# Kernel tuning notes

Measured on AMD Instinct MI355X. Metric: run time of the kernel, lower is better.

The kernel has to match this reference:

```python
import jax, jax.numpy as jnp
import numpy as np
import math

H = 16
D_MODEL = 1024
D_K = D_MODEL // H


def setup_inputs() -> dict:
    key = jax.random.key(0)
    ks = jax.random.split(key, 11)
    B, S = 2, 2048
    scale = 1.0 / math.sqrt(D_MODEL)
    inp = {
        "query": jax.random.normal(ks[0], (B, S, D_MODEL), dtype=jnp.float32),
        "key": jax.random.normal(ks[1], (B, S, D_MODEL), dtype=jnp.float32),
        "value": jax.random.normal(ks[2], (B, S, D_MODEL), dtype=jnp.float32),
        # torch nn.Linear convention: W is [out_features, in_features]
        "Wq": jax.random.normal(ks[3], (D_MODEL, D_MODEL), dtype=jnp.float32) * scale,
        "bq": jnp.zeros((D_MODEL,), dtype=jnp.float32),
        "Wk": jax.random.normal(ks[4], (D_MODEL, D_MODEL), dtype=jnp.float32) * scale,
        "bk": jnp.zeros((D_MODEL,), dtype=jnp.float32),
        "Wv": jax.random.normal(ks[5], (D_MODEL, D_MODEL), dtype=jnp.float32) * scale,
        "bv": jnp.zeros((D_MODEL,), dtype=jnp.float32),
        "Wo": jax.random.normal(ks[6], (D_MODEL, D_MODEL), dtype=jnp.float32) * scale,
        "bo": jnp.zeros((D_MODEL,), dtype=jnp.float32),
    }
    return inp


def _split_heads(x):
    # [b, s, h*d_k] -> [b, h, s, d_k]
    b, s, _ = x.shape
    return x.reshape(b, s, H, D_K).transpose(0, 2, 1, 3)


def reference(query, key, value, Wq, bq, Wk, bk, Wv, bv, Wo, bo):
    q = _split_heads(query @ Wq.T + bq)
    k = _split_heads(key @ Wk.T + bk)
    v = _split_heads(value @ Wv.T + bv)
    # scaled dot-product attention, full L x L scores per head
    scores = jnp.einsum("bhqd,bhkd->bhqk", q, k) / math.sqrt(D_K)
    attn = jax.nn.softmax(scores, axis=-1)
    ctx = jnp.einsum("bhqk,bhkd->bhqd", attn, v)  # [b, h, s, d_k]
    b, h, s, d = ctx.shape
    ctx = ctx.transpose(0, 2, 1, 3).reshape(b, s, h * d)
    return ctx @ Wo.T + bo
```

## Files before the change

kernel.cpp:

```cpp
#include <hip/hip_runtime.h>

typedef unsigned int u32;
typedef unsigned short u16;
typedef __attribute__((ext_vector_type(8))) short short8;
typedef __attribute__((ext_vector_type(4))) float f32x4;
typedef __attribute__((ext_vector_type(2))) u32 u32x2;
typedef __attribute__((ext_vector_type(4))) u32 u32x4;

#define DEV __device__ __forceinline__

DEV u16 f2bf(float f) {
  u32 u = __builtin_bit_cast(u32, f);
  u = (u + 0x7FFFu + ((u >> 16) & 1u)) >> 16;
  return (u16)u;
}

DEV float fexp2(float x) {
#if __has_builtin(__builtin_amdgcn_exp2f)
  return __builtin_amdgcn_exp2f(x);
#else
  return exp2f(x);
#endif
}

DEV u32 cvt_pk_bf16(float lo, float hi) {
  u32 r;
  asm("v_cvt_pk_bf16_f32 %0, %1, %2" : "=v"(r) : "v"(lo), "v"(hi));
  return r;
}

DEV void llds16(const void* g, void* lds) {
  __builtin_amdgcn_global_load_lds(
      (const __attribute__((address_space(1))) u32*)g,
      (__attribute__((address_space(3))) u32*)lds, 16, 0, 0);
}

struct CvtW {
  const float* src[4];
  u16* dst[4];
};

__global__ void cvt_w(CvtW cw) {
  int i = blockIdx.x * blockDim.x + threadIdx.x;
  int seg = i >> 17;
  size_t off = ((size_t)(i & 131071)) * 8;
  const f32x4* p = (const f32x4*)(cw.src[seg] + off);
  f32x4 a = p[0], b = p[1];
  u32x4 o;
  o[0] = cvt_pk_bf16(a[0], a[1]);
  o[1] = cvt_pk_bf16(a[2], a[3]);
  o[2] = cvt_pk_bf16(b[0], b[1]);
  o[3] = cvt_pk_bf16(b[2], b[3]);
  *(u32x4*)(cw.dst[seg] + off) = o;
}

struct GemmArgs {
  const void* A[3];
  const u16* W[3];
  const float* bias[3];
  void* C[3];
  float scale[3];
};

template <int BM, int BN, int WAVES_M, int OUT_BF16, int NB_M, int A_F32>
__global__ __launch_bounds__(256, 2) void gemm_bt(GemmArgs ga) {
  constexpr int K = 1024, N = 1024;
  constexpr int WAVES_N = 4 / WAVES_M;
  constexpr int WM = BM / WAVES_M, WN = BN / WAVES_N;
  constexpr int AM = WM / 16, AN = WN / 16;

  __shared__ u16 lsA[BM * 32];
  __shared__ u16 lsB[BN * 32];

  const u32 orig = blockIdx.x;
  const u32 nid = (orig & 7u) * (gridDim.x >> 3) + (orig >> 3);
  const int bn = (int)(nid & 7u);
  const int bm = (int)((nid >> 3) % (u32)NB_M);
  const int z = (int)((nid >> 3) / (u32)NB_M);

  const u16* __restrict__ W = ga.W[z];
  const int tid = threadIdx.x;
  const int l = tid & 63, w = tid >> 6;
  const int lg = l >> 4, lr = l & 15;
  const int wm = w / WAVES_N, wn = w % WAVES_N;

  f32x4 acc[AM][AN];
#pragma unroll
  for (int i = 0; i < AM; ++i)
#pragma unroll
    for (int j = 0; j < AN; ++j) acc[i][j] = (f32x4){0.f, 0.f, 0.f, 0.f};

  for (int k0 = 0; k0 < K; k0 += 32) {
    __syncthreads();
    if constexpr (A_F32) {
      const float* __restrict__ Af = (const float*)ga.A[z];
#pragma unroll
      for (int i = 0; i < BN / 64; ++i) {
        u32 sb = (u32)(w * (BN / 64) + i) * 1024;
        u32 lb = sb + l * 16;
        u32 row = lb >> 6, colS = (lb & 63) >> 1;
        llds16(W + (size_t)(bn * BN + row) * K + k0 + colS, (char*)lsB + sb);
      }
      {
        constexpr int TPR = 256 / BM;
        int row = tid / TPR, kh = tid % TPR;
        const f32x4* src = (const f32x4*)(Af + (size_t)(bm * BM + row) * K + k0 + kh * 16);
        f32x4 f0 = src[0], f1 = src[1], f2 = src[2], f3 = src[3];
        u32x4 o0, o1;
        o0[0] = cvt_pk_bf16(f0[0], f0[1]); o0[1] = cvt_pk_bf16(f0[2], f0[3]);
        o0[2] = cvt_pk_bf16(f1[0], f1[1]); o0[3] = cvt_pk_bf16(f1[2], f1[3]);
        o1[0] = cvt_pk_bf16(f2[0], f2[1]); o1[1] = cvt_pk_bf16(f2[2], f2[3]);
        o1[2] = cvt_pk_bf16(f3[0], f3[1]); o1[3] = cvt_pk_bf16(f3[2], f3[3]);
        char* dst = (char*)lsA + row * 64 + kh * 32;
        *(u32x4*)dst = o0;
        *(u32x4*)(dst + 16) = o1;
      }
    } else {
      const u16* __restrict__ A = (const u16*)ga.A[z];
      constexpr int SEGS = (BM + BN) / 16;
      constexpr int PW = SEGS / 4;
#pragma unroll
      for (int i = 0; i < PW; ++i) {
        int s = w * PW + i;
        if (s < BM / 16) {
          u32 sb = s * 1024;
          u32 lb = sb + l * 16;
          u32 row = lb >> 6, colS = (lb & 63) >> 1;
          llds16(A + (size_t)(bm * BM + row) * K + k0 + colS, (char*)lsA + sb);
        } else {
          u32 sb = (u32)(s - BM / 16) * 1024;
          u32 lb = sb + l * 16;
          u32 row = lb >> 6, colS = (lb & 63) >> 1;
          llds16(W + (size_t)(bn * BN + row) * K + k0 + colS, (char*)lsB + sb);
        }
      }
    }
    __syncthreads();
    short8 af[AM], bf[AN];
#pragma unroll
    for (int i = 0; i < AM; ++i)
      af[i] = *(const short8*)&lsA[(wm * WM + i * 16 + lr) * 32 + lg * 8];
#pragma unroll
    for (int j = 0; j < AN; ++j)
      bf[j] = *(const short8*)&lsB[(wn * WN + j * 16 + lr) * 32 + lg * 8];
#pragma unroll
    for (int i = 0; i < AM; ++i)
#pragma unroll
      for (int j = 0; j < AN; ++j)
        acc[i][j] = __builtin_amdgcn_mfma_f32_16x16x32_bf16(af[i], bf[j], acc[i][j], 0, 0, 0);
  }

  const float sc = ga.scale[z];
  const float* __restrict__ bias = ga.bias[z];
#pragma unroll
  for (int j = 0; j < AN; ++j) {
    int col = bn * BN + wn * WN + j * 16 + lr;
    float bv = bias[col];
#pragma unroll
    for (int i = 0; i < AM; ++i) {
      int row0 = bm * BM + wm * WM + i * 16 + lg * 4;
#pragma unroll
      for (int r = 0; r < 4; ++r) {
        float v = (acc[i][j][r] + bv) * sc;
        if constexpr (OUT_BF16)
          ((u16*)ga.C[z])[(size_t)(row0 + r) * N + col] = f2bf(v);
        else
          ((float*)ga.C[z])[(size_t)(row0 + r) * N + col] = v;
      }
    }
  }
}

__global__ __launch_bounds__(256, 2) void attn_fwd(
    const u16* __restrict__ Q, const u16* __restrict__ Kp,
    const u16* __restrict__ V, u16* __restrict__ O) {
  constexpr int S = 2048, LD = 1024;
  __shared__ u16 Kt[4][64 * 64];
  __shared__ u16 Vt[4][64 * 64];
  const int tid = threadIdx.x;
  const int l = tid & 63, w = tid >> 6;
  const int lg = l >> 4, lr = l & 15;

  const u32 orig = blockIdx.x;
  const u32 nid = (orig & 7u) * 64u + (orig >> 3);
  const int qt = (int)(nid & 15u);
  const int h = (int)((nid >> 4) & 15u);
  const int b = (int)(nid >> 8);

  const size_t base = ((size_t)b * S) * LD + h * 64;
  const int q0 = qt * 128 + w * 32;

  short8 qf[2][2];
#pragma unroll
  for (int g = 0; g < 2; ++g)
#pragma unroll
    for (int c = 0; c < 2; ++c)
      qf[g][c] = *(const short8*)&Q[base + (size_t)(q0 + g * 16 + lr) * LD + c * 32 + lg * 8];

  f32x4 acc[2][4];
#pragma unroll
  for (int g = 0; g < 2; ++g)
#pragma unroll
    for (int i = 0; i < 4; ++i) acc[g][i] = (f32x4){0.f, 0.f, 0.f, 0.f};
  float lsum[2] = {0.f, 0.f};

  const int m = tid & 31;
  const int kp0 = m * 2;
  const int key0 = ((m & 16) << 1) + ((m & 2) << 3) + (((m >> 2) & 3) << 2) + ((m & 1) << 1);
  const int vd0 = (tid >> 5) * 8;

#define KSTAGE(T)                                                               \
  {                                                                             \
    _Pragma("unroll") for (int i_ = 0; i_ < 2; ++i_) {                          \
      u32 sb = (u32)(w * 2 + i_) * 1024;                                        \
      u32 lb = sb + l * 16;                                                     \
      u32 key = lb >> 7;                                                        \
      u32 inner = (lb & 127) ^ ((key & 7) << 4);                                \
      llds16(Kp + base + (size_t)((T) * 64 + key) * LD + (inner >> 1),          \
             (char*)Kt[(T) & 3] + sb);                                          \
    }                                                                           \
  }
#define VLOAD(T, VA, VB)                                                        \
  {                                                                             \
    VA = *(const short8*)&V[base + (size_t)((T) * 64 + key0) * LD + vd0];       \
    VB = *(const short8*)&V[base + (size_t)((T) * 64 + key0 + 1) * LD + vd0];   \
  }
#define VWRITE(T, VA, VB)                                                       \
  {                                                                             \
    _Pragma("unroll") for (int jj = 0; jj < 8; ++jj) {                          \
      u32 pv = (u32)(u16)(VA)[jj] | ((u32)(u16)(VB)[jj] << 16);                 \
      u32 addr = (u32)((vd0 + jj) * 128 + kp0 * 2) ^ ((u32)jj << 4);            \
      *(u32*)((char*)Vt[(T) & 3] + addr) = pv;                                  \
    }                                                                           \
  }
#define QK(T, SV)                                                               \
  {                                                                             \
    __builtin_amdgcn_s_setprio(1);                                              \
    _Pragma("unroll") for (int ks = 0; ks < 4; ++ks) {                          \
      u32 a0 = (u32)(((ks * 16 + lr) * 128 + lg * 16) ^ ((lr & 7) << 4));       \
      short8 kf0 = *(const short8*)((const char*)Kt[(T) & 3] + a0);             \
      short8 kf1 = *(const short8*)((const char*)Kt[(T) & 3] + (a0 ^ 64));      \
      _Pragma("unroll") for (int g = 0; g < 2; ++g) {                           \
        f32x4 s_ = (f32x4){0.f, 0.f, 0.f, 0.f};                                 \
        s_ = __builtin_amdgcn_mfma_f32_16x16x32_bf16(kf0, qf[g][0], s_, 0, 0, 0); \
        s_ = __builtin_amdgcn_mfma_f32_16x16x32_bf16(kf1, qf[g][1], s_, 0, 0, 0); \
        SV[g][ks] = s_;                                                         \
      }                                                                         \
    }                                                                           \
    __builtin_amdgcn_s_setprio(0);                                              \
  }
#define SM(SV, PK)                                                              \
  {                                                                             \
    _Pragma("unroll") for (int g = 0; g < 2; ++g) {                             \
      _Pragma("unroll") for (int ks = 0; ks < 4; ++ks) {                        \
        float e0 = fexp2(SV[g][ks][0]), e1 = fexp2(SV[g][ks][1]);               \
        float e2 = fexp2(SV[g][ks][2]), e3 = fexp2(SV[g][ks][3]);               \
        lsum[g] += (e0 + e1) + (e2 + e3);                                       \
        PK[g][ks * 2 + 0] = cvt_pk_bf16(e0, e1);                                \
        PK[g][ks * 2 + 1] = cvt_pk_bf16(e2, e3);                                \
      }                                                                         \
    }                                                                           \
  }
#define PV(T, PK)                                                               \
  {                                                                             \
    __builtin_amdgcn_s_setprio(1);                                              \
    _Pragma("unroll") for (int ds = 0; ds < 4; ++ds) {                          \
      _Pragma("unroll") for (int c = 0; c < 2; ++c) {                           \
        u32 va_ = (u32)(((ds * 16 + lr) * 128 + c * 64 + lg * 16) ^ ((lr & 7) << 4)); \
        short8 vf = *(const short8*)((const char*)Vt[(T) & 3] + va_);           \
        _Pragma("unroll") for (int g = 0; g < 2; ++g) {                         \
          u32x4 pc = {PK[g][c * 4 + 0], PK[g][c * 4 + 1], PK[g][c * 4 + 2], PK[g][c * 4 + 3]}; \
          short8 pf = __builtin_bit_cast(short8, pc);                           \
          acc[g][ds] = __builtin_amdgcn_mfma_f32_16x16x32_bf16(vf, pf, acc[g][ds], 0, 0, 0); \
        }                                                                       \
      }                                                                         \
    }                                                                           \
    __builtin_amdgcn_s_setprio(0);                                              \
  }
#define ITER(t, SVC, SVN, VCA, VCB, VNA, VNB)                                   \
  {                                                                             \
    if ((t) < 30) { VLOAD((t) + 2, VNA, VNB); KSTAGE((t) + 2); }                \
    if ((t) < 31) QK((t) + 1, SVN);                                             \
    u32 pk_[2][8];                                                              \
    SM(SVC, pk_);                                                               \
    if ((t) < 31) VWRITE((t) + 1, VCA, VCB);                                    \
    PV(t, pk_);                                                                 \
    __syncthreads();                                                            \
  }

  f32x4 svA[2][4], svB[2][4];
  short8 vaA, vbA, vaB, vbB;

  VLOAD(0, vaB, vbB); KSTAGE(0);
  VLOAD(1, vaA, vbA); KSTAGE(1);
  VWRITE(0, vaB, vbB);
  __syncthreads();
  QK(0, svA);

  for (int tt = 0; tt < 16; ++tt) {
    ITER(2 * tt, svA, svB, vaA, vbA, vaB, vbB);
    ITER(2 * tt + 1, svB, svA, vaB, vbB, vaA, vbA);
  }

#pragma unroll
  for (int g = 0; g < 2; ++g) {
    lsum[g] += __shfl_xor(lsum[g], 16);
    lsum[g] += __shfl_xor(lsum[g], 32);
  }
#pragma unroll
  for (int g = 0; g < 2; ++g) {
    float inv = __builtin_amdgcn_rcpf(lsum[g]);
#pragma unroll
    for (int ds = 0; ds < 4; ++ds) {
      u32x2 ov;
      ov[0] = cvt_pk_bf16(acc[g][ds][0] * inv, acc[g][ds][1] * inv);
      ov[1] = cvt_pk_bf16(acc[g][ds][2] * inv, acc[g][ds][3] * inv);
      *(u32x2*)&O[base + (size_t)(q0 + g * 16 + lr) * LD + ds * 16 + lg * 4] = ov;
    }
  }
#undef KSTAGE
#undef VLOAD
#undef VWRITE
#undef QK
#undef SM
#undef PV
#undef ITER
}

extern "C" void kernel_launch(void* const* d_in, const int* in_sizes, int n_in,
                              void* d_out, int out_size, void* d_ws, size_t ws_size,
                              hipStream_t stream) {
  constexpr size_t SZ_X = 4096ull * 1024;
  constexpr size_t SZ_W = 1024ull * 1024;
  const float* bq = (const float*)d_in[4];
  const float* bk = (const float*)d_in[6];
  const float* bv = (const float*)d_in[8];
  const float* bo = (const float*)d_in[10];

  char* ws = (char*)d_ws;
  u16* wqb = (u16*)ws;
  u16* wkb = wqb + SZ_W;
  u16* wvb = wkb + SZ_W;
  u16* wob = wvb + SZ_W;
  u16* Qp = wob + SZ_W;
  u16* Kp = Qp + SZ_X;
  u16* Vp = Kp + SZ_X;
  u16* Cx = Vp + SZ_X;

  CvtW cw;
  cw.src[0] = (const float*)d_in[3]; cw.dst[0] = wqb;
  cw.src[1] = (const float*)d_in[5]; cw.dst[1] = wkb;
  cw.src[2] = (const float*)d_in[7]; cw.dst[2] = wvb;
  cw.src[3] = (const float*)d_in[9]; cw.dst[3] = wob;
  cvt_w<<<dim3(2048), 256, 0, stream>>>(cw);

  GemmArgs g1;
  g1.A[0] = d_in[0]; g1.A[1] = d_in[1]; g1.A[2] = d_in[2];
  g1.W[0] = wqb; g1.W[1] = wkb; g1.W[2] = wvb;
  g1.bias[0] = bq; g1.bias[1] = bk; g1.bias[2] = bv;
  g1.C[0] = Qp; g1.C[1] = Kp; g1.C[2] = Vp;
  g1.scale[0] = 0.18033688011112042f;
  g1.scale[1] = 1.f; g1.scale[2] = 1.f;
  gemm_bt<128, 128, 2, 1, 32, 1><<<dim3(768), 256, 0, stream>>>(g1);

  attn_fwd<<<dim3(512), 256, 0, stream>>>(Qp, Kp, Vp, Cx);

  GemmArgs g2 = {};
  g2.A[0] = Cx; g2.W[0] = wob; g2.bias[0] = bo; g2.C[0] = d_out; g2.scale[0] = 1.f;
  gemm_bt<64, 128, 1, 0, 64, 0><<<dim3(512), 256, 0, stream>>>(g2);
}
```

Before: 131.2 us.

## Swizzle GEMM LDS layout and register-prefetch fp32 A tiles one step ahead

Applies an XOR swizzle on the 16-byte column chunks of the A and B LDS tiles, keyed on the row, on both the direct-to-LDS loads and the fragment reads, so the MFMA fragment loads hit fewer bank conflicts. In the fp32-A path, the next K-step's A values are loaded into registers before the current step converts and stores its own, so global-load latency overlaps the MFMA work. This raises register pressure, and the fp32 path now assumes a fixed 2-segment-per-wave layout, i.e. BM=128 and BN=128.

Result: faster. 123.6 us (-5.8%).

```diff
diff --git a/kernel.cpp b/kernel.cpp
--- a/kernel.cpp
+++ b/kernel.cpp
@@ -90,65 +90,105 @@
 #pragma unroll
     for (int j = 0; j < AN; ++j) acc[i][j] = (f32x4){0.f, 0.f, 0.f, 0.f};
 
-  for (int k0 = 0; k0 < K; k0 += 32) {
-    __syncthreads();
-    if constexpr (A_F32) {
-      const float* __restrict__ Af = (const float*)ga.A[z];
-#pragma unroll
-      for (int i = 0; i < BN / 64; ++i) {
-        u32 sb = (u32)(w * (BN / 64) + i) * 1024;
-        u32 lb = sb + l * 16;
-        u32 row = lb >> 6, colS = (lb & 63) >> 1;
-        llds16(W + (size_t)(bn * BN + row) * K + k0 + colS, (char*)lsB + sb);
-      }
-      {
-        constexpr int TPR = 256 / BM;
-        int row = tid / TPR, kh = tid % TPR;
-        const f32x4* src = (const f32x4*)(Af + (size_t)(bm * BM + row) * K + k0 + kh * 16);
-        f32x4 f0 = src[0], f1 = src[1], f2 = src[2], f3 = src[3];
-        u32x4 o0, o1;
-        o0[0] = cvt_pk_bf16(f0[0], f0[1]); o0[1] = cvt_pk_bf16(f0[2], f0[3]);
-        o0[2] = cvt_pk_bf16(f1[0], f1[1]); o0[3] = cvt_pk_bf16(f1[2], f1[3]);
-        o1[0] = cvt_pk_bf16(f2[0], f2[1]); o1[1] = cvt_pk_bf16(f2[2], f2[3]);
-        o1[2] = cvt_pk_bf16(f3[0], f3[1]); o1[3] = cvt_pk_bf16(f3[2], f3[3]);
-        char* dst = (char*)lsA + row * 64 + kh * 32;
-        *(u32x4*)dst = o0;
-        *(u32x4*)(dst + 16) = o1;
-      }
-    } else {
-      const u16* __restrict__ A = (const u16*)ga.A[z];
-      constexpr int SEGS = (BM + BN) / 16;
-      constexpr int PW = SEGS / 4;
+#define WDMA_SWZ(NSEG)                                                          \
+  {                                                                             \
+    _Pragma("unroll") for (int i_ = 0; i_ < (NSEG); ++i_) {                     \
+      u32 sb = (u32)(w * (NSEG) + i_) * 1024;                                   \
+      u32 lbw = sb + l * 16;                                                    \
+      u32 row = lbw >> 6;                                                       \
+      u32 colB = (lbw & 63) ^ ((row & 3) << 4);                                 \
+      llds16(W + (size_t)(bn * BN + row) * K + k0 + (colB >> 1),                \
+             (char*)lsB + sb);                                                  \
+    }                                                                           \
+  }
+#define FRAG_MFMA()                                                             \
+  {                                                                             \
+    short8 af[AM], bf[AN];                                                      \
+    _Pragma("unroll") for (int i = 0; i < AM; ++i) {                            \
+      u32 ar = (u32)(wm * WM + i * 16 + lr);                                    \
+      af[i] = *(const short8*)((const char*)lsA + ar * 64 +                     \
+                               ((u32)(lg * 16) ^ ((ar & 3) << 4)));             \
+    }                                                                           \
+    _Pragma("unroll") for (int j = 0; j < AN; ++j) {                            \
+      u32 br = (u32)(wn * WN + j * 16 + lr);                                    \
+      bf[j] = *(const short8*)((const char*)lsB + br * 64 +                     \
+                               ((u32)(lg * 16) ^ ((br & 3) << 4)));             \
+    }                                                                           \
+    _Pragma("unroll") for (int i = 0; i < AM; ++i)                              \
+    _Pragma("unroll") for (int j = 0; j < AN; ++j)                              \
+      acc[i][j] = __builtin_amdgcn_mfma_f32_16x16x32_bf16(af[i], bf[j],         \
+                                                          acc[i][j], 0, 0, 0); \
+  }
+
+  if constexpr (A_F32) {
+    const float* __restrict__ Af = (const float*)ga.A[z];
+    const u32 lb0 = (u32)(w * 2 + 0) * 1024 + l * 16;
+    const u32 lb1 = (u32)(w * 2 + 1) * 1024 + l * 16;
+    const u32 sw0 = lb0 ^ (((lb0 >> 6) & 3) << 4);
+    const u32 sw1 = lb1 ^ (((lb1 >> 6) & 3) << 4);
+    const float* src0 = Af + (size_t)(bm * BM + (lb0 >> 6)) * K + ((lb0 & 63) >> 1);
+    const float* src1 = Af + (size_t)(bm * BM + (lb1 >> 6)) * K + ((lb1 & 63) >> 1);
+
+    f32x4 cA0, cA1, cB0, cB1, nA0, nA1, nB0, nB1;
+    cA0 = *(const f32x4*)src0; cA1 = *(const f32x4*)(src0 + 4);
+    cB0 = *(const f32x4*)src1; cB1 = *(const f32x4*)(src1 + 4);
+
+#define GSTEP(K0, CA0, CA1, CB0, CB1, NA0, NA1, NB0, NB1)                       \
+  {                                                                             \
+    const int k0 = (K0);                                                        \
+    __syncthreads();                                                            \
+    if (k0 + 32 < K) {          \
+      NA0 = *(const f32x4*)(src0 + k0 + 32); NA1 = *(const f32x4*)(src0 + k0 + 36); \
+      NB0 = *(const f32x4*)(src1 + k0 + 32); NB1 = *(const f32x4*)(src1 + k0 + 36); \
+    }                                                                           \
+    WDMA_SWZ(2);                                                                \
+    {                                                                           \
+      u32x4 o;                                                                  \
+      o[0] = cvt_pk_bf16(CA0[0], CA0[1]); o[1] = cvt_pk_bf16(CA0[2], CA0[3]);   \
+      o[2] = cvt_pk_bf16(CA1[0], CA1[1]); o[3] = cvt_pk_bf16(CA1[2], CA1[3]);   \
+      *(u32x4*)((char*)lsA + sw0) = o;                                          \
+      o[0] = cvt_pk_bf16(CB0[0], CB0[1]); o[1] = cvt_pk_bf16(CB0[2], CB0[3]);   \
+      o[2] = cvt_pk_bf16(CB1[0], CB1[1]); o[3] = cvt_pk_bf16(CB1[2], CB1[3]);   \
+      *(u32x4*)((char*)lsA + sw1) = o;                                          \
+    }                                                                           \
+    __syncthreads();                                                            \
+    FRAG_MFMA();                                                                \
+  }
+
+    for (int kk = 0; kk < K; kk += 64) {
+      GSTEP(kk, cA0, cA1, cB0, cB1, nA0, nA1, nB0, nB1);
+      GSTEP(kk + 32, nA0, nA1, nB0, nB1, cA0, cA1, cB0, cB1);
+    }
+#undef GSTEP
+  } else {
+    const u16* __restrict__ A = (const u16*)ga.A[z];
+    constexpr int SEGS = (BM + BN) / 16;
+    constexpr int PW = SEGS / 4;
+    for (int k0 = 0; k0 < K; k0 += 32) {
+      __syncthreads();
 #pragma unroll
       for (int i = 0; i < PW; ++i) {
         int s = w * PW + i;
         if (s < BM / 16) {
           u32 sb = s * 1024;
           u32 lb = sb + l * 16;
-          u32 row = lb >> 6, colS = (lb & 63) >> 1;
-          llds16(A + (size_t)(bm * BM + row) * K + k0 + colS, (char*)lsA + sb);
+          u32 row = lb >> 6;
+          u32 colB = (lb & 63) ^ ((row & 3) << 4);
+          llds16(A + (size_t)(bm * BM + row) * K + k0 + (colB >> 1), (char*)lsA + sb);
         } else {
           u32 sb = (u32)(s - BM / 16) * 1024;
           u32 lb = sb + l * 16;
-          u32 row = lb >> 6, colS = (lb & 63) >> 1;
-          llds16(W + (size_t)(bn * BN + row) * K + k0 + colS, (char*)lsB + sb);
+          u32 row = lb >> 6;
+          u32 colB = (lb & 63) ^ ((row & 3) << 4);
+          llds16(W + (size_t)(bn * BN + row) * K + k0 + (colB >> 1), (char*)lsB + sb);
         }
       }
+      __syncthreads();
+      FRAG_MFMA();
     }
-    __syncthreads();
-    short8 af[AM], bf[AN];
-#pragma unroll
-    for (int i = 0; i < AM; ++i)
-      af[i] = *(const short8*)&lsA[(wm * WM + i * 16 + lr) * 32 + lg * 8];
-#pragma unroll
-    for (int j = 0; j < AN; ++j)
-      bf[j] = *(const short8*)&lsB[(wn * WN + j * 16 + lr) * 32 + lg * 8];
-#pragma unroll
-    for (int i = 0; i < AM; ++i)
-#pragma unroll
-      for (int j = 0; j < AN; ++j)
-        acc[i][j] = __builtin_amdgcn_mfma_f32_16x16x32_bf16(af[i], bf[j], acc[i][j], 0, 0, 0);
-  }
+  }
+#undef WDMA_SWZ
+#undef FRAG_MFMA
 
   const float sc = ga.scale[z];
   const float* __restrict__ bias = ga.bias[z];
```

## Double K tile to 64 with XOR-swizzled LDS and register-prefetched fp32 A

Applied to the files above, without the earlier changes.

Raises the GEMM K-step from 32 to 64, which halves the number of barrier pairs per tile. LDS rows are now 128 bytes with an XOR swizzle on the row index to avoid bank conflicts. In the fp32-input path, the next A tile is loaded into registers while the current one is converted and computed on, hiding global load latency. This doubles LDS use and raises register pressure, which may reduce occupancy at 2 blocks per CU.

Measured after the change: 127.6 us. -2.7%, faster.

```diff
diff --git a/kernel.cpp b/kernel.cpp
--- a/kernel.cpp
+++ b/kernel.cpp
@@ -69,8 +69,8 @@
   constexpr int WM = BM / WAVES_M, WN = BN / WAVES_N;
   constexpr int AM = WM / 16, AN = WN / 16;
 
-  __shared__ u16 lsA[BM * 32];
-  __shared__ u16 lsB[BN * 32];
+  __shared__ u16 lsA[BM * 64];
+  __shared__ u16 lsB[BN * 64];
 
   const u32 orig = blockIdx.x;
   const u32 nid = (orig & 7u) * (gridDim.x >> 3) + (orig >> 3);
@@ -90,65 +90,103 @@
 #pragma unroll
     for (int j = 0; j < AN; ++j) acc[i][j] = (f32x4){0.f, 0.f, 0.f, 0.f};
 
-  for (int k0 = 0; k0 < K; k0 += 32) {
-    __syncthreads();
-    if constexpr (A_F32) {
-      const float* __restrict__ Af = (const float*)ga.A[z];
-#pragma unroll
-      for (int i = 0; i < BN / 64; ++i) {
-        u32 sb = (u32)(w * (BN / 64) + i) * 1024;
-        u32 lb = sb + l * 16;
-        u32 row = lb >> 6, colS = (lb & 63) >> 1;
-        llds16(W + (size_t)(bn * BN + row) * K + k0 + colS, (char*)lsB + sb);
-      }
-      {
-        constexpr int TPR = 256 / BM;
-        int row = tid / TPR, kh = tid % TPR;
-        const f32x4* src = (const f32x4*)(Af + (size_t)(bm * BM + row) * K + k0 + kh * 16);
-        f32x4 f0 = src[0], f1 = src[1], f2 = src[2], f3 = src[3];
-        u32x4 o0, o1;
-        o0[0] = cvt_pk_bf16(f0[0], f0[1]); o0[1] = cvt_pk_bf16(f0[2], f0[3]);
-        o0[2] = cvt_pk_bf16(f1[0], f1[1]); o0[3] = cvt_pk_bf16(f1[2], f1[3]);
-        o1[0] = cvt_pk_bf16(f2[0], f2[1]); o1[1] = cvt_pk_bf16(f2[2], f2[3]);
-        o1[2] = cvt_pk_bf16(f3[0], f3[1]); o1[3] = cvt_pk_bf16(f3[2], f3[3]);
-        char* dst = (char*)lsA + row * 64 + kh * 32;
-        *(u32x4*)dst = o0;
-        *(u32x4*)(dst + 16) = o1;
-      }
-    } else {
-      const u16* __restrict__ A = (const u16*)ga.A[z];
-      constexpr int SEGS = (BM + BN) / 16;
-      constexpr int PW = SEGS / 4;
+#define STAGE_SEG(MAT, ROWBASE, LSX, SB, K0)                                    \
+  {                                                                             \
+    u32 lb = (u32)(SB) + l * 16;                                                \
+    u32 row = lb >> 7;                                                          \
+    u32 inner = (lb & 127) ^ ((row & 7) << 4);                                  \
+    llds16((MAT) + (size_t)((ROWBASE) + row) * K + (K0) + (inner >> 1),         \
+           (char*)(LSX) + (SB));                                                \
+  }
+#define FRAG_MFMA()                                                             \
+  {                                                                             \
+    _Pragma("unroll") for (int c = 0; c < 2; ++c) {                             \
+      short8 af[AM], bf[AN];                                                    \
+      _Pragma("unroll") for (int i = 0; i < AM; ++i) {                          \
+        u32 ar = (u32)(wm * WM + i * 16 + lr);                                  \
+        af[i] = *(const short8*)((const char*)lsA + ar * 128 +                  \
+                 (((u32)(c * 64) + (u32)(lg * 16)) ^ ((ar & 7) << 4)));         \
+      }                                                                         \
+      _Pragma("unroll") for (int j = 0; j < AN; ++j) {                          \
+        u32 br = (u32)(wn * WN + j * 16 + lr);                                  \
+        bf[j] = *(const short8*)((const char*)lsB + br * 128 +                  \
+                 (((u32)(c * 64) + (u32)(lg * 16)) ^ ((br & 7) << 4)));         \
+      }                                                                         \
+      _Pragma("unroll") for (int i = 0; i < AM; ++i)                            \
+      _Pragma("unroll") for (int j = 0; j < AN; ++j)                            \
+        acc[i][j] = __builtin_amdgcn_mfma_f32_16x16x32_bf16(af[i], bf[j],       \
+                                                            acc[i][j], 0, 0, 0); \
+    }                                                                           \
+  }
+
+  if constexpr (A_F32) {
+    const float* __restrict__ Af = (const float*)ga.A[z];
+    const float* srcA[4];
+    u32 lbA[4];
+#pragma unroll
+    for (int i = 0; i < 4; ++i) {
+      u32 lb = (u32)(w * 4 + i) * 1024 + l * 16;
+      u32 row = lb >> 7;
+      u32 inner = (lb & 127) ^ ((row & 7) << 4);
+      lbA[i] = lb;
+      srcA[i] = Af + (size_t)(bm * BM + row) * K + (inner >> 1);
+    }
+    f32x4 ca[4][2], na[4][2];
+#pragma unroll
+    for (int i = 0; i < 4; ++i) {
+      ca[i][0] = *(const f32x4*)(srcA[i]);
+      ca[i][1] = *(const f32x4*)(srcA[i] + 4);
+    }
+
+#define GSTEP(K0, CUR, NXT)                                                     \
+  {                                                                             \
+    __syncthreads();                                                            \
+    _Pragma("unroll") for (int i = 0; i < 4; ++i)                               \
+      STAGE_SEG(W, bn * BN, lsB, (w * 4 + i) * 1024, (K0));                     \
+    _Pragma("unroll") for (int i = 0; i < 4; ++i) {                             \
+      u32x4 o;                                                                  \
+      o[0] = cvt_pk_bf16(CUR[i][0][0], CUR[i][0][1]);                           \
+      o[1] = cvt_pk_bf16(CUR[i][0][2], CUR[i][0][3]);                           \
+      o[2] = cvt_pk_bf16(CUR[i][1][0], CUR[i][1][1]);                           \
+      o[3] = cvt_pk_bf16(CUR[i][1][2], CUR[i][1][3]);                           \
+      *(u32x4*)((char*)lsA + lbA[i]) = o;                                       \
+    }                                                                           \
+    if ((K0) + 64 < K) {                                                        \
+      _Pragma("unroll") for (int i = 0; i < 4; ++i) {                           \
+        NXT[i][0] = *(const f32x4*)(srcA[i] + (K0) + 64);                       \
+        NXT[i][1] = *(const f32x4*)(srcA[i] + (K0) + 68);                       \
+      }                                                                         \
+    }                                                                           \
+    __syncthreads();                                                            \
+    FRAG_MFMA();                                                                \
+  }
+
+    for (int kk = 0; kk < K; kk += 128) {
+      GSTEP(kk, ca, na);
+      GSTEP(kk + 64, na, ca);
+    }
+#undef GSTEP
+  } else {
+    const u16* __restrict__ A = (const u16*)ga.A[z];
+    constexpr int SEGS = (BM + BN) / 8;
+    constexpr int PW = SEGS / 4;
+    for (int k0 = 0; k0 < K; k0 += 64) {
+      __syncthreads();
 #pragma unroll
       for (int i = 0; i < PW; ++i) {
         int s = w * PW + i;
-        if (s < BM / 16) {
-          u32 sb = s * 1024;
-          u32 lb = sb + l * 16;
-          u32 row = lb >> 6, colS = (lb & 63) >> 1;
-          llds16(A + (size_t)(bm * BM + row) * K + k0 + colS, (char*)lsA + sb);
+        if (s < BM / 8) {
+          STAGE_SEG(A, bm * BM, lsA, s * 1024, k0);
         } else {
-          u32 sb = (u32)(s - BM / 16) * 1024;
-          u32 lb = sb + l * 16;
-          u32 row = lb >> 6, colS = (lb & 63) >> 1;
-          llds16(W + (size_t)(bn * BN + row) * K + k0 + colS, (char*)lsB + sb);
+          STAGE_SEG(W, bn * BN, lsB, (s - BM / 8) * 1024, k0);
         }
       }
-    }
-    __syncthreads();
-    short8 af[AM], bf[AN];
-#pragma unroll
-    for (int i = 0; i < AM; ++i)
-      af[i] = *(const short8*)&lsA[(wm * WM + i * 16 + lr) * 32 + lg * 8];
-#pragma unroll
-    for (int j = 0; j < AN; ++j)
-      bf[j] = *(const short8*)&lsB[(wn * WN + j * 16 + lr) * 32 + lg * 8];
-#pragma unroll
-    for (int i = 0; i < AM; ++i)
-#pragma unroll
-      for (int j = 0; j < AN; ++j)
-        acc[i][j] = __builtin_amdgcn_mfma_f32_16x16x32_bf16(af[i], bf[j], acc[i][j], 0, 0, 0);
-  }
+      __syncthreads();
+      FRAG_MFMA();
+    }
+  }
+#undef STAGE_SEG
+#undef FRAG_MFMA
 
   const float sc = ga.scale[z];
   const float* __restrict__ bias = ga.bias[z];
```
